# Kernel tuning notes

Measured on AMD Instinct MI355X. Metric: run time of the kernel, lower is better.

Reference implementation:

```python
import jax, jax.numpy as jnp
import numpy as np

B, M, GRID = 4, 8192, 32          # batches, points per batch, voxel grid side
N = B * M
K = 8                              # knn neighbors (includes self at dist 0)
C_IN, C_OUT, H = 8, 8, 128
KEYB = 64                          # hash base (coords shifted +1 stay in [0,33])
EPS = 1e-5


def setup_inputs() -> dict:
    rng = np.random.default_rng(0)
    # unique occupied voxels per batch (ME SparseTensor requires unique coords)
    cs = []
    for b in range(B):
        lin = rng.choice(GRID ** 3, size=M, replace=False)
        x, y, z = lin // (GRID * GRID), (lin // GRID) % GRID, lin % GRID
        cs.append(np.stack([np.full(M, b), x, y, z], axis=1))
    coords = jnp.asarray(np.concatenate(cs, axis=0).astype(np.int32))  # [N,4]

    key = jax.random.key(0)
    ks = jax.random.split(key, 4)
    feats = jax.random.normal(ks[0], (N, C_IN), jnp.float32)
    w1 = jax.random.normal(ks[1], ((K + 1) * C_IN, H), jnp.float32) * 0.05  # 1x1 conv
    g1 = jnp.ones((H,), jnp.float32)
    b1 = jnp.zeros((H,), jnp.float32)
    w3 = jax.random.normal(ks[2], (27, H, H), jnp.float32) * 0.02          # 3^3 sparse conv
    g2 = jnp.ones((H,), jnp.float32)
    b2 = jnp.zeros((H,), jnp.float32)
    w_out = jax.random.normal(ks[3], (H, 2 * C_OUT), jnp.float32) * 0.05   # 1x1 conv
    return dict(coords=coords, feats=feats, w1=w1, g1=g1, b1=b1,
                w3=w3, g2=g2, b2=b2, w_out=w_out)


def _knn_idx(coords):
    # per-batch brute-force kNN on xyz (batch column segments the search)
    xyz = coords[:, 1:].astype(jnp.float32).reshape(B, M, 3)
    d2 = jnp.sum((xyz[:, :, None, :] - xyz[:, None, :, :]) ** 2, -1)  # [B,M,M]
    _, idx = jax.lax.top_k(-d2, K)                                     # [B,M,K]
    return (idx + (jnp.arange(B) * M)[:, None, None]).reshape(N, K)


def _bn(x, g, b):
    mu = jnp.mean(x, axis=0)
    var = jnp.var(x, axis=0)
    return (x - mu) * jax.lax.rsqrt(var + EPS) * g + b


def reference(coords, feats, w1, g1, b1, w3, g2, b2, w_out):
    # --- kNN gather-and-build: [center || k neighbor feats] -> (k+1)*C_in ---
    nbr = _knn_idx(coords)                                        # [N,K] int
    combined = jnp.concatenate([feats[:, None, :], feats[nbr]], axis=1)
    combined = combined.reshape(N, (K + 1) * C_IN)
    # --- neighbor_processor: 1x1 conv + BN + ReLU ---
    h = jax.nn.relu(_bn(combined @ w1, g1, b1))                   # [N,H]
    # --- context_predictor conv k=3: gather inputs at coord+offset via hash ---
    c = coords[:, 1:] + 1                                         # shift so offsets stay >= 0
    keys = ((coords[:, 0] * KEYB + c[:, 0]) * KEYB + c[:, 1]) * KEYB + c[:, 2]
    order = jnp.argsort(keys)
    skeys = keys[order]
    offs = jnp.stack(jnp.meshgrid(*([jnp.arange(-1, 2)] * 3), indexing='ij'),
                     axis=-1).reshape(27, 3)                      # {-1,0,1}^3
    okey = (offs[:, 0] * KEYB + offs[:, 1]) * KEYB + offs[:, 2]   # [27]
    q = keys[None, :] + okey[:, None]                             # [27,N]
    pos = jnp.clip(jnp.searchsorted(skeys, q), 0, N - 1)
    valid = skeys[pos] == q                                       # [27,N]
    j = order[pos]                                                # [27,N]
    gathered = jnp.where(valid[..., None], h[j], 0.0)             # [27,N,H]
    h2 = jnp.einsum('onc,ocd->nd', gathered, w3)                  # [N,H]
    h2 = jax.nn.relu(_bn(h2, g2, b2))
    # --- final 1x1 conv -> mean/scale ---
    return h2 @ w_out                                             # [N, 2*C_OUT]
```

## Files before the change

kernel.cpp:

```cpp
#include <hip/hip_runtime.h>
#include <hip/hip_bf16.h>

#define B_   4
#define M_   8192
#define N_   32768
#define H_   128
#define EPS_ 1e-5f
#define TBL  1048576
#define GUARD 8192

typedef short short8 __attribute__((ext_vector_type(8)));
typedef float f32x4  __attribute__((ext_vector_type(4)));

__global__ __launch_bounds__(256) void prep_pack_kernel(const int* __restrict__ coords,
                                                        int* __restrict__ table,
                                                        int* __restrict__ packed,
                                                        int* __restrict__ keyb,
                                                        const float* __restrict__ w3,
                                                        ushort* __restrict__ w3f,
                                                        float* __restrict__ gsum1,
                                                        float* __restrict__ gsum2,
                                                        int* __restrict__ flagcnt,
                                                        unsigned int* __restrict__ hbz) {
    int bid = blockIdx.x, tid = threadIdx.x;
    if (bid < 128) {
        int n = bid * 256 + tid;
        int b = coords[4*n+0], x = coords[4*n+1], y = coords[4*n+2], z = coords[4*n+3];
        packed[n] = (x << 10) | (y << 5) | z;
        int key = ((b*64 + x+1)*64 + y+1)*64 + (z+1);
        keyb[n] = key;
        table[key] = n;
        if (bid < 8)  gsum1[bid*256 + tid] = 0.f;
        if (bid == 0) gsum2[tid] = 0.f;
        if (bid == 8 && tid < 64) hbz[tid] = 0u;
        if (bid == 9 && tid == 0) *flagcnt = 0;
        return;
    }
    int t = (bid - 128) * 256 + tid;
    int lane = t & 63;
    int ct   = (t >> 6) & 7;
    int ks   = (t >> 9) & 3;
    int o    = t >> 11;
    int quad = lane >> 4, l15 = lane & 15;
    int n = ct*16 + l15;
    const float* src = w3 + o*16384;
    ushort out8[8];
#pragma unroll
    for (int j = 0; j < 8; ++j) {
        int c = ks*32 + quad*8 + j;
        float v = src[c*128 + n];
        __hip_bfloat16 bv = __float2bfloat16(v);
        ushort u; __builtin_memcpy(&u, &bv, 2);
        out8[j] = u;
    }
    *(uint4*)&w3f[t*8] = *(uint4*)out8;
}

__global__ __launch_bounds__(256) void knn_window_kernel(const int* __restrict__ table,
                                                         const int* __restrict__ keyb,
                                                         int* __restrict__ nbr,
                                                         int* __restrict__ flagcnt,
                                                         int* __restrict__ flaglist) {
    __shared__ int okey_sh[93], d2_sh[93];
    __shared__ int tops[256 * 8];
    __shared__ int ncnt;
    int tid = threadIdx.x;
    if (tid == 0) ncnt = 0;
    __syncthreads();
    if (tid < 125) {
        int dx = tid / 25 - 2, rr = tid % 25, dy = rr / 5 - 2, dz = rr % 5 - 2;
        int d2 = dx*dx + dy*dy + dz*dz;
        if (d2 <= 8) {
            int p = atomicAdd(&ncnt, 1);
            okey_sh[p] = dx * 4096 + dy * 64 + dz;
            d2_sh[p]   = d2;
        }
    }
    __syncthreads();

    int q   = blockIdx.x * 64 + (tid >> 2);
    int sub = tid & 3;
    int kb  = keyb[q];

    int top[8];
#pragma unroll
    for (int k = 0; k < 8; ++k) top[k] = 0x7FFFFFFF;

    int base = sub * 24;
    int cnt  = (sub == 3) ? 21 : 24;
    for (int i = 0; i < cnt; ++i) {
        int idx = base + i;
        int j = table[kb + okey_sh[idx]];
        if (j >= 0) {
            int key = (d2_sh[idx] << 13) | (j & 8191);
            if (key < top[7]) {
#pragma unroll
                for (int k = 7; k >= 1; --k)
                    top[k] = (key < top[k]) ? max(key, top[k-1]) : top[k];
                top[0] = min(key, top[0]);
            }
        }
    }
#pragma unroll
    for (int k = 0; k < 8; ++k) tops[tid*8 + k] = top[k];
    __syncthreads();

    if (sub == 0) {
        const int* L = &tops[tid*8];
        int ia0 = 0, ia1 = 0, ia2 = 0, ia3 = 0;
        int res[8];
#pragma unroll
        for (int k = 0; k < 8; ++k) {
            int v0 = L[ia0], v1 = L[8 + ia1], v2 = L[16 + ia2], v3 = L[24 + ia3];
            int m01 = min(v0, v1), m23 = min(v2, v3);
            int m = min(m01, m23);
            res[k] = m;
            if (m == v0) ++ia0; else if (m == v1) ++ia1;
            else if (m == v2) ++ia2; else ++ia3;
        }
        int bb = q & ~(M_-1);
        if ((res[7] >> 13) <= 8) {
#pragma unroll
            for (int k = 0; k < 8; ++k) nbr[q*8 + k] = bb + (res[k] & 8191);
        } else {
            int pos = atomicAdd(flagcnt, 1);
            flaglist[pos] = q;
        }
    }
}

__global__ __launch_bounds__(256) void knn_bf_kernel(const int* __restrict__ packed,
                                                     const int* __restrict__ flagcnt,
                                                     const int* __restrict__ flaglist,
                                                     int* __restrict__ nbr) {
    __shared__ int tops[256 * 8];
    int tid = threadIdx.x;
    int cnt = *flagcnt;
    for (int f = blockIdx.x; f < cnt; f += gridDim.x) {
        int n = flaglist[f];
        int bb = n & ~(M_-1);
        int p = packed[n];
        int qx = (p >> 10) & 31, qy = (p >> 5) & 31, qz = p & 31;
        int top[8];
#pragma unroll
        for (int k = 0; k < 8; ++k) top[k] = 0x7FFFFFFF;
        for (int j = tid; j < M_; j += 256) {
            int c = packed[bb + j];
            int dx = qx - ((c >> 10) & 31);
            int dy = qy - ((c >> 5) & 31);
            int dz = qz - (c & 31);
            int d2 = dx*dx + dy*dy + dz*dz;
            int key = (d2 << 13) | j;
            if (key < top[7]) {
#pragma unroll
                for (int k = 7; k >= 1; --k)
                    top[k] = (key < top[k]) ? max(key, top[k-1]) : top[k];
                top[0] = min(key, top[0]);
            }
        }
#pragma unroll
        for (int k = 0; k < 8; ++k) tops[tid*8 + k] = top[k];
        __syncthreads();
        for (int stride = 128; stride >= 1; stride >>= 1) {
            if (tid < stride) {
                int* A  = &tops[tid*8];
                int* Bp = &tops[(tid+stride)*8];
                int r[8]; int ia = 0, ib = 0;
#pragma unroll
                for (int k = 0; k < 8; ++k) {
                    int a = A[ia], b2 = Bp[ib];
                    if (a <= b2) { r[k] = a; ++ia; } else { r[k] = b2; ++ib; }
                }
#pragma unroll
                for (int k = 0; k < 8; ++k) A[k] = r[k];
            }
            __syncthreads();
        }
        if (tid == 0) {
#pragma unroll
            for (int k = 0; k < 8; ++k) nbr[n*8 + k] = bb + (tops[k] & 8191);
        }
        __syncthreads();
    }
}

__global__ __launch_bounds__(256) void h1_kernel(const float* __restrict__ feats,
                                                 const int* __restrict__ nbr,
                                                 const float* __restrict__ w1,
                                                 float* __restrict__ hpre,
                                                 float* __restrict__ gsum1) {
    __shared__ float comb[16][72];
    __shared__ float ssum[256], ssq[256];
    int tid = threadIdx.x;
    int rowbase = blockIdx.x * 16;
    if (tid < 144) {
        int r = tid / 9, s = tid % 9;
        int grow = rowbase + r;
        int idx = (s == 0) ? grow : nbr[grow*8 + (s-1)];
        const float4* f = (const float4*)(feats + idx * 8);
        float4 a = f[0], b = f[1];
        float* dp = &comb[r][s*8];
        dp[0]=a.x; dp[1]=a.y; dp[2]=a.z; dp[3]=a.w;
        dp[4]=b.x; dp[5]=b.y; dp[6]=b.z; dp[7]=b.w;
    }
    __syncthreads();
    int c = tid & 127, rh = tid >> 7;
    float acc[8];
#pragma unroll
    for (int i = 0; i < 8; ++i) acc[i] = 0.f;
    for (int s = 0; s < 72; ++s) {
        float w = w1[s*128 + c];
#pragma unroll
        for (int i = 0; i < 8; ++i)
            acc[i] += comb[rh*8 + i][s] * w;
    }
    float s = 0.f, q = 0.f;
#pragma unroll
    for (int i = 0; i < 8; ++i) {
        hpre[(rowbase + rh*8 + i)*128 + c] = acc[i];
        s += acc[i]; q += acc[i]*acc[i];
    }
    ssum[tid] = s; ssq[tid] = q;
    __syncthreads();
    if (tid < 128) {
        float S = ssum[tid] + ssum[tid+128];
        float Q = ssq[tid]  + ssq[tid+128];
        float* g = gsum1 + (blockIdx.x & 7) * 256;
        atomicAdd(&g[tid], S);
        atomicAdd(&g[128 + tid], Q);
    }
}

__global__ __launch_bounds__(256) void bnrelu_bf16_kernel(const float* __restrict__ x,
                                                          const float* __restrict__ gsum1,
                                                          const float* __restrict__ g1,
                                                          const float* __restrict__ b1,
                                                          ushort* __restrict__ y) {
    __shared__ float sc[128], sh[128];
    int tid = threadIdx.x;
    if (tid < 128) {
        float s = 0.f, q = 0.f;
#pragma unroll
        for (int r = 0; r < 8; ++r) {
            s += gsum1[r*256 + tid];
            q += gsum1[r*256 + 128 + tid];
        }
        float mu  = s / (float)N_;
        float var = q / (float)N_ - mu*mu;
        float inv = rsqrtf(var + EPS_);
        float scv = inv * g1[tid];
        sc[tid] = scv;
        sh[tid] = b1[tid] - mu * scv;
    }
    __syncthreads();
    int i = blockIdx.x * 256 + tid;
    float4 v = ((const float4*)x)[i];
    int c = (i * 4) & 127;
    v.x = fmaxf(0.f, v.x*sc[c]   + sh[c]);
    v.y = fmaxf(0.f, v.y*sc[c+1] + sh[c+1]);
    v.z = fmaxf(0.f, v.z*sc[c+2] + sh[c+2]);
    v.w = fmaxf(0.f, v.w*sc[c+3] + sh[c+3]);
    ushort o[4];
#pragma unroll
    for (int k = 0; k < 4; ++k) {
        float f = (&v.x)[k];
        __hip_bfloat16 bv = __float2bfloat16(f);
        __builtin_memcpy(&o[k], &bv, 2);
    }
    ((ushort4*)y)[i] = make_ushort4(o[0], o[1], o[2], o[3]);
}

#define CONV3_LDS 145408
__global__ __launch_bounds__(512) void conv3_mfma_kernel(const ushort* __restrict__ hb,
                                                         const ushort* __restrict__ w3f,
                                                         const int* __restrict__ table,
                                                         const int* __restrict__ keyb,
                                                         float* __restrict__ h2,
                                                         float* __restrict__ gsum) {
    extern __shared__ char smem_raw[];
    ushort* Asb = (ushort*)smem_raw;
    ushort* Bsb = (ushort*)(smem_raw + 65536);
    int*    jsh = (int*)(smem_raw + 131072);
    int*    kbsh= (int*)(smem_raw + 144896);

    int tid = threadIdx.x;
    int lane = tid & 63, wid = tid >> 6;
    int quad = lane >> 4, l15 = lane & 15;
    int bid = blockIdx.x;
    int swz = (bid & 7) * 32 + (bid >> 3);
    int rowbase = swz * 128;
    int wr = wid >> 1;
    int cb = (wid & 1) * 4;

    if (tid < 128) kbsh[tid] = keyb[rowbase + tid];
    __syncthreads();
    for (int t = tid; t < 27*128; t += 512) {
        int o = t >> 7, r = t & 127;
        int dx = o/9 - 1, dy = (o/3)%3 - 1, dz = o%3 - 1;
        jsh[t] = table[kbsh[r] + dx*4096 + dy*64 + dz];
    }
    __syncthreads();

#pragma unroll
    for (int i = 0; i < 4; ++i) {
        int flat = i*512 + tid;
        int r = flat >> 4, cp = flat & 15;
        int j = jsh[r];
        const ushort* asrc = hb + j*128 + ((cp ^ (r & 15)) << 3);
        __builtin_amdgcn_global_load_lds(
            (const __attribute__((address_space(1))) unsigned int*)asrc,
            (__attribute__((address_space(3))) unsigned int*)&Asb[flat << 3],
            16, 0, 0);
        __builtin_amdgcn_global_load_lds(
            (const __attribute__((address_space(1))) unsigned int*)(w3f + (flat << 3)),
            (__attribute__((address_space(3))) unsigned int*)&Bsb[flat << 3],
            16, 0, 0);
    }
    __syncthreads();

    f32x4 acc[2][4];
#pragma unroll
    for (int i = 0; i < 2; ++i)
#pragma unroll
        for (int c = 0; c < 4; ++c)
            acc[i][c] = (f32x4){0.f, 0.f, 0.f, 0.f};

    int cur = 0;
#pragma unroll 1
    for (int o = 0; o < 27; ++o) {
        if (o < 26) {
            int obase = (o + 1) << 7;
            const ushort* wsrc = w3f + ((o + 1) << 14);
            int dst = (cur ^ 1) * 16384;
#pragma unroll
            for (int i = 0; i < 4; ++i) {
                int flat = i*512 + tid;
                int r = flat >> 4, cp = flat & 15;
                int j = jsh[obase + r];
                const ushort* asrc = hb + j*128 + ((cp ^ (r & 15)) << 3);
                __builtin_amdgcn_global_load_lds(
                    (const __attribute__((address_space(1))) unsigned int*)asrc,
                    (__attribute__((address_space(3))) unsigned int*)&Asb[dst + (flat << 3)],
                    16, 0, 0);
                __builtin_amdgcn_global_load_lds(
                    (const __attribute__((address_space(1))) unsigned int*)(wsrc + (flat << 3)),
                    (__attribute__((address_space(3))) unsigned int*)&Bsb[dst + (flat << 3)],
                    16, 0, 0);
            }
        }
        const ushort* Ac = Asb + cur*16384;
        const ushort* Bc = Bsb + cur*16384;
#pragma unroll
        for (int ks = 0; ks < 4; ++ks) {
            short8 af[2], bfr[4];
#pragma unroll
            for (int i = 0; i < 2; ++i) {
                int lr = wr*32 + i*16 + l15;
                int chunk = (ks*4 + quad) ^ l15;
                af[i] = *(const short8*)&Ac[lr*128 + chunk*8];
            }
#pragma unroll
            for (int c = 0; c < 4; ++c)
                bfr[c] = *(const short8*)&Bc[((ks*8 + cb + c)*64 + lane) << 3];
#pragma unroll
            for (int i = 0; i < 2; ++i)
#pragma unroll
                for (int c = 0; c < 4; ++c)
                    acc[i][c] = __builtin_amdgcn_mfma_f32_16x16x32_bf16(af[i], bfr[c], acc[i][c], 0, 0, 0);
        }
        __syncthreads();
        cur ^= 1;
    }

    float s[4], q[4];
#pragma unroll
    for (int c = 0; c < 4; ++c) { s[c] = 0.f; q[c] = 0.f; }
#pragma unroll
    for (int i = 0; i < 2; ++i)
#pragma unroll
        for (int c = 0; c < 4; ++c)
#pragma unroll
            for (int r = 0; r < 4; ++r) {
                int row = rowbase + wr*32 + i*16 + quad*4 + r;
                int col = (cb + c)*16 + l15;
                float v = acc[i][c][r];
                h2[row*128 + col] = v;
                s[c] += v; q[c] += v*v;
            }
    float* red = (float*)smem_raw;
    if (tid < 256) red[tid] = 0.f;
    __syncthreads();
#pragma unroll
    for (int c = 0; c < 4; ++c) {
        int col = (cb + c)*16 + l15;
        atomicAdd(&red[col], s[c]);
        atomicAdd(&red[128 + col], q[c]);
    }
    __syncthreads();
    if (tid < 256) atomicAdd(&gsum[tid], red[tid]);
}

__global__ __launch_bounds__(256) void out_kernel(const float* __restrict__ h2,
                                                  const float* __restrict__ wout,
                                                  const float* __restrict__ gsum2,
                                                  const float* __restrict__ g2,
                                                  const float* __restrict__ b2,
                                                  float* __restrict__ out) {
    __shared__ float hrow[128][129];
    __shared__ float wsh[2048];
    __shared__ float sc[128], sh[128];
    int tid = threadIdx.x;
    if (tid < 128) {
        float s = gsum2[tid], q = gsum2[128 + tid];
        float mu  = s / (float)N_;
        float var = q / (float)N_ - mu*mu;
        float inv = rsqrtf(var + EPS_);
        float scv = inv * g2[tid];
        sc[tid] = scv;
        sh[tid] = b2[tid] - mu * scv;
    }
#pragma unroll
    for (int i = 0; i < 8; ++i) wsh[i*256 + tid] = wout[i*256 + tid];
    __syncthreads();

    int rowbase = blockIdx.x * 128;
#pragma unroll
    for (int i = 0; i < 16; ++i) {
        int flat = i*256 + tid;
        int row = flat >> 5, c4 = (flat & 31) * 4;
        float4 v = *(const float4*)&h2[(rowbase + row)*128 + c4];
        float4 scv = *(const float4*)&sc[c4];
        float4 shv = *(const float4*)&sh[c4];
        hrow[row][c4+0] = fmaxf(0.f, fmaf(v.x, scv.x, shv.x));
        hrow[row][c4+1] = fmaxf(0.f, fmaf(v.y, scv.y, shv.y));
        hrow[row][c4+2] = fmaxf(0.f, fmaf(v.z, scv.z, shv.z));
        hrow[row][c4+3] = fmaxf(0.f, fmaf(v.w, scv.w, shv.w));
    }
    __syncthreads();

    int row = tid >> 1, dbase = (tid & 1) * 8;
    float acc[8];
#pragma unroll
    for (int k = 0; k < 8; ++k) acc[k] = 0.f;
    for (int c = 0; c < 128; ++c) {
        float hv = hrow[row][c];
        float4 w0 = *(const float4*)&wsh[c*16 + dbase];
        float4 w1 = *(const float4*)&wsh[c*16 + dbase + 4];
        acc[0] = fmaf(hv, w0.x, acc[0]);
        acc[1] = fmaf(hv, w0.y, acc[1]);
        acc[2] = fmaf(hv, w0.z, acc[2]);
        acc[3] = fmaf(hv, w0.w, acc[3]);
        acc[4] = fmaf(hv, w1.x, acc[4]);
        acc[5] = fmaf(hv, w1.y, acc[5]);
        acc[6] = fmaf(hv, w1.z, acc[6]);
        acc[7] = fmaf(hv, w1.w, acc[7]);
    }
    float* op = out + (rowbase + row)*16 + dbase;
    *(float4*)op       = (float4){acc[0], acc[1], acc[2], acc[3]};
    *(float4*)(op + 4) = (float4){acc[4], acc[5], acc[6], acc[7]};
}

extern "C" void kernel_launch(void* const* d_in, const int* in_sizes, int n_in,
                              void* d_out, int out_size, void* d_ws, size_t ws_size,
                              hipStream_t stream) {
    const int*   coords = (const int*)d_in[0];
    const float* feats  = (const float*)d_in[1];
    const float* w1     = (const float*)d_in[2];
    const float* g1     = (const float*)d_in[3];
    const float* b1     = (const float*)d_in[4];
    const float* w3     = (const float*)d_in[5];
    const float* g2     = (const float*)d_in[6];
    const float* b2     = (const float*)d_in[7];
    const float* wout   = (const float*)d_in[8];
    float* out = (float*)d_out;

    char* ws = (char*)d_ws;
    int*    table_base = (int*)(ws);
    int*    table   = table_base + GUARD;
    int*    packed  = (int*)(ws + (4352u<<10));
    int*    keyb    = (int*)(ws + (4608u<<10));
    int*    nbr     = (int*)(ws + (4864u<<10));
    int*    flagcnt = (int*)(ws + (5888u<<10));
    int*    flaglist= (int*)(ws + (5892u<<10));
    float*  gsum2   = (float*)(ws + (6416u<<10));
    float*  gsum1   = (float*)(ws + (6420u<<10));
    ushort* w3f     = (ushort*)(ws + (6656u<<10));
    ushort* hb      = (ushort*)(ws + (7680u<<10));
    float*  h       = (float*)(ws + (15872u<<10));
    float*  h2      = h;

    static bool conv3_attr_set = false;
    if (!conv3_attr_set) {
        hipFuncSetAttribute(reinterpret_cast<const void*>(&conv3_mfma_kernel),
                            hipFuncAttributeMaxDynamicSharedMemorySize, CONV3_LDS);
        conv3_attr_set = true;
    }

    hipMemsetAsync(table_base, 0xFF, (TBL + GUARD) * sizeof(int), stream);
    prep_pack_kernel <<<344, 256, 0, stream>>>(coords, table, packed, keyb, w3, w3f,
                                               gsum1, gsum2, flagcnt,
                                               (unsigned int*)(hb - 128));
    knn_window_kernel<<<N_/64, 256, 0, stream>>>(table, keyb, nbr, flagcnt, flaglist);
    knn_bf_kernel    <<<256, 256, 0, stream>>>(packed, flagcnt, flaglist, nbr);
    h1_kernel        <<<N_/16, 256, 0, stream>>>(feats, nbr, w1, h, gsum1);
    bnrelu_bf16_kernel<<<(N_*H_/4)/256, 256, 0, stream>>>(h, gsum1, g1, b1, hb);
    conv3_mfma_kernel<<<N_/128, 512, CONV3_LDS, stream>>>(hb, w3f, table, keyb, h2, gsum2);
    out_kernel       <<<N_/128, 256, 0, stream>>>(h2, wout, gsum2, g2, b2, out);
}
```

Baseline: 194.3 us.

## Fuse kNN window search and brute-force fallback into one kernel

Merges the windowed kNN kernel and the brute-force fallback kernel into one launch. Flagged queries are now kept in a per-block shared list and resolved in the same block, replacing the global atomic flag list and its counter initialisation. The table lookups are also fully unrolled into a register array, with three padded sentinel offsets so every lane does 24 loads, which raises memory-level parallelism. The cost is that any block holding flagged queries runs a serial 8192-point scan per query, which can leave some blocks as long stragglers, and register pressure goes up.

```diff
diff --git a/kernel.cpp b/kernel.cpp
--- a/kernel.cpp
+++ b/kernel.cpp
@@ -20,7 +20,6 @@
                                                         ushort* __restrict__ w3f,
                                                         float* __restrict__ gsum1,
                                                         float* __restrict__ gsum2,
-                                                        int* __restrict__ flagcnt,
                                                         unsigned int* __restrict__ hbz) {
     int bid = blockIdx.x, tid = threadIdx.x;
     if (bid < 128) {
@@ -33,7 +32,6 @@
         if (bid < 8)  gsum1[bid*256 + tid] = 0.f;
         if (bid == 0) gsum2[tid] = 0.f;
         if (bid == 8 && tid < 64) hbz[tid] = 0u;
-        if (bid == 9 && tid == 0) *flagcnt = 0;
         return;
     }
     int t = (bid - 128) * 256 + tid;
@@ -56,16 +54,16 @@
     *(uint4*)&w3f[t*8] = *(uint4*)out8;
 }
 
-__global__ __launch_bounds__(256) void knn_window_kernel(const int* __restrict__ table,
-                                                         const int* __restrict__ keyb,
-                                                         int* __restrict__ nbr,
-                                                         int* __restrict__ flagcnt,
-                                                         int* __restrict__ flaglist) {
-    __shared__ int okey_sh[93], d2_sh[93];
+__global__ __launch_bounds__(256) void knn_kernel(const int* __restrict__ table,
+                                                  const int* __restrict__ keyb,
+                                                  const int* __restrict__ packed,
+                                                  int* __restrict__ nbr) {
+    __shared__ int okey_sh[96], d2_sh[96];
     __shared__ int tops[256 * 8];
-    __shared__ int ncnt;
+    __shared__ int flagq[64];
+    __shared__ int ncnt, fln;
     int tid = threadIdx.x;
-    if (tid == 0) ncnt = 0;
+    if (tid == 0) { ncnt = 0; fln = 0; }
     __syncthreads();
     if (tid < 125) {
         int dx = tid / 25 - 2, rr = tid % 25, dy = rr / 5 - 2, dz = rr % 5 - 2;
@@ -77,22 +75,27 @@
         }
     }
     __syncthreads();
+    if (tid < 3) { okey_sh[93 + tid] = 0; d2_sh[93 + tid] = 9; }
+    __syncthreads();
 
     int q   = blockIdx.x * 64 + (tid >> 2);
     int sub = tid & 3;
     int kb  = keyb[q];
 
+    int jv[24];
+    int base = sub * 24;
+#pragma unroll
+    for (int i = 0; i < 24; ++i)
+        jv[i] = table[kb + okey_sh[base + i]];
+
     int top[8];
 #pragma unroll
     for (int k = 0; k < 8; ++k) top[k] = 0x7FFFFFFF;
-
-    int base = sub * 24;
-    int cnt  = (sub == 3) ? 21 : 24;
-    for (int i = 0; i < cnt; ++i) {
-        int idx = base + i;
-        int j = table[kb + okey_sh[idx]];
+#pragma unroll
+    for (int i = 0; i < 24; ++i) {
+        int j = jv[i];
         if (j >= 0) {
-            int key = (d2_sh[idx] << 13) | (j & 8191);
+            int key = (d2_sh[base + i] << 13) | (j & 8191);
             if (key < top[7]) {
 #pragma unroll
                 for (int k = 7; k >= 1; --k)
@@ -123,27 +126,21 @@
 #pragma unroll
             for (int k = 0; k < 8; ++k) nbr[q*8 + k] = bb + (res[k] & 8191);
         } else {
-            int pos = atomicAdd(flagcnt, 1);
-            flaglist[pos] = q;
-        }
-    }
-}
-
-__global__ __launch_bounds__(256) void knn_bf_kernel(const int* __restrict__ packed,
-                                                     const int* __restrict__ flagcnt,
-                                                     const int* __restrict__ flaglist,
-                                                     int* __restrict__ nbr) {
-    __shared__ int tops[256 * 8];
-    int tid = threadIdx.x;
-    int cnt = *flagcnt;
-    for (int f = blockIdx.x; f < cnt; f += gridDim.x) {
-        int n = flaglist[f];
+            int pos = atomicAdd(&fln, 1);
+            flagq[pos] = q;
+        }
+    }
+    __syncthreads();
+
+    int cnt = fln;
+    for (int f = 0; f < cnt; ++f) {
+        int n = flagq[f];
         int bb = n & ~(M_-1);
         int p = packed[n];
         int qx = (p >> 10) & 31, qy = (p >> 5) & 31, qz = p & 31;
-        int top[8];
-#pragma unroll
-        for (int k = 0; k < 8; ++k) top[k] = 0x7FFFFFFF;
+        int bt[8];
+#pragma unroll
+        for (int k = 0; k < 8; ++k) bt[k] = 0x7FFFFFFF;
         for (int j = tid; j < M_; j += 256) {
             int c = packed[bb + j];
             int dx = qx - ((c >> 10) & 31);
@@ -151,15 +148,15 @@
             int dz = qz - (c & 31);
             int d2 = dx*dx + dy*dy + dz*dz;
             int key = (d2 << 13) | j;
-            if (key < top[7]) {
+            if (key < bt[7]) {
 #pragma unroll
                 for (int k = 7; k >= 1; --k)
-                    top[k] = (key < top[k]) ? max(key, top[k-1]) : top[k];
-                top[0] = min(key, top[0]);
+                    bt[k] = (key < bt[k]) ? max(key, bt[k-1]) : bt[k];
+                bt[0] = min(key, bt[0]);
             }
         }
 #pragma unroll
-        for (int k = 0; k < 8; ++k) tops[tid*8 + k] = top[k];
+        for (int k = 0; k < 8; ++k) tops[tid*8 + k] = bt[k];
         __syncthreads();
         for (int stride = 128; stride >= 1; stride >>= 1) {
             if (tid < stride) {
@@ -480,8 +477,6 @@
     int*    packed  = (int*)(ws + (4352u<<10));
     int*    keyb    = (int*)(ws + (4608u<<10));
     int*    nbr     = (int*)(ws + (4864u<<10));
-    int*    flagcnt = (int*)(ws + (5888u<<10));
-    int*    flaglist= (int*)(ws + (5892u<<10));
     float*  gsum2   = (float*)(ws + (6416u<<10));
     float*  gsum1   = (float*)(ws + (6420u<<10));
     ushort* w3f     = (ushort*)(ws + (6656u<<10));
@@ -498,10 +493,8 @@
 
     hipMemsetAsync(table_base, 0xFF, (TBL + GUARD) * sizeof(int), stream);
     prep_pack_kernel <<<344, 256, 0, stream>>>(coords, table, packed, keyb, w3, w3f,
-                                               gsum1, gsum2, flagcnt,
-                                               (unsigned int*)(hb - 128));
-    knn_window_kernel<<<N_/64, 256, 0, stream>>>(table, keyb, nbr, flagcnt, flaglist);
-    knn_bf_kernel    <<<256, 256, 0, stream>>>(packed, flagcnt, flaglist, nbr);
+                                               gsum1, gsum2, (unsigned int*)(hb - 128));
+    knn_kernel       <<<N_/64, 256, 0, stream>>>(table, keyb, packed, nbr);
     h1_kernel        <<<N_/16, 256, 0, stream>>>(feats, nbr, w1, h, gsum1);
     bnrelu_bf16_kernel<<<(N_*H_/4)/256, 256, 0, stream>>>(h, gsum1, g1, b1, hb);
     conv3_mfma_kernel<<<N_/128, 512, CONV3_LDS, stream>>>(hb, w3f, table, keyb, h2, gsum2);
```

New measurement: 220.8 us. 13.6% more time.
